# Kernel tuning notes

Measured on AMD Instinct MI355X. Metric: run time of the kernel, lower is better.

Reference implementation:

```python
import jax, jax.numpy as jnp
import numpy as np
from math import factorial as fact

L, P, T, CIN, COUT, N = 4, 5, 15, 32, 32, 1000


def _cg(j1, m1, j2, m2, J, M):
    # Clebsch-Gordan coefficient <j1 m1 j2 m2 | J M> (integer args, Racah formula)
    if m1 + m2 != M or not (abs(j1 - j2) <= J <= j1 + j2):
        return 0.0
    if abs(m1) > j1 or abs(m2) > j2 or abs(M) > J:
        return 0.0
    pre = (2.0 * J + 1.0) * fact(J + j1 - j2) * fact(J - j1 + j2) * fact(j1 + j2 - J) / fact(j1 + j2 + J + 1)
    pre *= fact(J + M) * fact(J - M) * fact(j1 - m1) * fact(j1 + m1) * fact(j2 - m2) * fact(j2 + m2)
    s = 0.0
    for k in range(0, j1 + j2 - J + 1):
        d = (k, j1 + j2 - J - k, j1 - m1 - k, j2 + m2 - k, J - j2 + m1 + k, J - j1 - m2 + k)
        if min(d) < 0:
            continue
        den = 1.0
        for x in d:
            den *= fact(x)
        s += (-1.0) ** k / den
    return float(np.sqrt(pre) * s)


def _precompute(Ldeg):
    # Mirrors PrecomputingTensorsForConv6D
    tensors, coefs = [], []
    for l in range(Ldeg):
        for l1 in range(Ldeg):
            for l2 in range(abs(l - l1), min(Ldeg, l + l1 + 1)):
                coefs.append(8.0 * np.pi ** 2 / (2 * l1 + 1)
                             * np.sqrt((2 * l + 1) * (2 * l1 + 1) / (4.0 * np.pi * (2 * l2 + 1)))
                             * _cg(l, 0, l1, 0, l2, 0))
                T1 = np.zeros((l + 1, l1 + 1, l2 + 1)); T2 = np.zeros_like(T1); T3 = np.zeros_like(T1)
                for k in range(l + 1):
                    for k1 in range(l1 + 1):
                        if abs(k + k1) < l2 + 1:
                            T1[k, k1, k + k1] = _cg(l, k, l1, k1, l2, k + k1) * (-1) ** k1
                        if k1 > 0 and abs(k - k1) < l2 + 1:
                            if k - k1 >= 0:
                                T2[k, k1, k - k1] = _cg(l, k, l1, -k1, l2, k - k1) * (-1) ** l1
                            else:
                                T3[k, k1, k1 - k] = (-1) ** (k1 - k) * (-1) ** (l1 + l2) * _cg(l, k, l1, -k1, l2, k - k1)
                tensors.append((jnp.asarray(T1, jnp.float32), jnp.asarray(T2, jnp.float32), jnp.asarray(T3, jnp.float32)))
    return tensors, np.asarray(coefs, np.float64)

_TENSORS, _COEFS = _precompute(L)


def setup_inputs() -> dict:
    key = jax.random.key(0)
    ks = iter(jax.random.split(key, 64))
    inp = {}
    for l in range(L):
        inp[f"in{l}_real"] = 0.1 * jax.random.normal(next(ks), (N, T, l + 1, P, CIN), jnp.float32)
        inp[f"in{l}_imag"] = 0.1 * jax.random.normal(next(ks), (N, T, l + 1, P, CIN), jnp.float32)
    for l in range(L):
        inp[f"w{l}_real"] = 0.05 * jax.random.normal(next(ks), (l + 1, T, P, CIN, COUT), jnp.float32)
        inp[f"w{l}_imag"] = 0.05 * jax.random.normal(next(ks), (l + 1, T, P, CIN, COUT), jnp.float32)
    for l in range(L):
        inp[f"b{l}_real"] = jax.random.uniform(next(ks), (1, l + 1, P, COUT), jnp.float32, -0.05, 0.05)
        inp[f"b{l}_imag"] = jax.random.uniform(next(ks), (1, l + 1, P, COUT), jnp.float32, -0.05, 0.05)
    return inp


def _forward(ins, ws_raw, bs_raw):
    # Mask imaginary parts: weight order-0 row (k=0) and bias degree-0 component are zeroed,
    # exactly as the temp_term masks in build().
    ws, bs = [], []
    for l in range(L):
        wmask = jnp.ones((l + 1, 1, 1, 1, 1), jnp.float32).at[0].set(0.0)
        ws += [ws_raw[2 * l], ws_raw[2 * l + 1] * wmask]
        bmask = jnp.ones((1, l + 1, 1, 1), jnp.float32).at[:, 0].set(0.0)
        bs += [bs_raw[2 * l], bs_raw[2 * l + 1] * bmask]
    outputs = []
    itr = 0
    for l in range(L):
        out_r = 0.0
        out_i = 0.0
        for l1 in range(L):
            for l2 in range(abs(l - l1), min(L, l + l1 + 1)):
                c = float(_COEFS[itr])
                T1, T2, T3 = _TENSORS[itr]
                xr, xi = ins[2 * l2], ins[2 * l2 + 1]      # [N, T, l2+1, P, Cin]
                wr, wi = ws[2 * l1], ws[2 * l1 + 1]        # [l1+1, T, P, Cin, Cout]
                # complex CG contraction -> [N, l+1, P, Cout]
                out_r = out_r + c * jnp.einsum('lmk,ntkpi,mtpij->nlpj', T1 + T2 + T3, xr, wr)
                out_r = out_r - c * jnp.einsum('lmk,ntkpi,mtpij->nlpj', T1 - T2 + T3, xi, wi)
                out_i = out_i + c * jnp.einsum('lmk,ntkpi,mtpij->nlpj', T1 - T2 - T3, xr, wi)
                out_i = out_i + c * jnp.einsum('lmk,ntkpi,mtpij->nlpj', T1 + T2 - T3, xi, wr)
                itr += 1
        outputs.append(out_r + bs[2 * l])
        outputs.append(out_i + bs[2 * l + 1])
    return tuple(outputs)


def reference(in0_real, in0_imag, in1_real, in1_imag, in2_real, in2_imag, in3_real, in3_imag,
              w0_real, w0_imag, w1_real, w1_imag, w2_real, w2_imag, w3_real, w3_imag,
              b0_real, b0_imag, b1_real, b1_imag, b2_real, b2_imag, b3_real, b3_imag):
    ins = [in0_real, in0_imag, in1_real, in1_imag, in2_real, in2_imag, in3_real, in3_imag]
    ws = [w0_real, w0_imag, w1_real, w1_imag, w2_real, w2_imag, w3_real, w3_imag]
    bs = [b0_real, b0_imag, b1_real, b1_imag, b2_real, b2_imag, b3_real, b3_imag]
    return _forward(ins, ws, bs)
```

## Files before the change

kernel.cpp:

```cpp
#include <hip/hip_runtime.h>
#include <hip/hip_bf16.h>

#define NB   1000
#define NPAD 1024
#define TT   15
#define PP   5
#define CI   32
#define CO   32
#define KDIM 9600
#define MDIM 640
#define NCHUNK 300
#define NCOL   20
#define TABN  16384
#define KSTEPS 150
#define WTELEMS 1536000
#define WTRX_BLOCKS 300
#define TAB_BLOCKS (TABN / 256)
#define XSLOTS 6000000
#define PADSLOTS 144000
#define XCVT_BLOCKS 24001

typedef __attribute__((ext_vector_type(8))) short          bf16x8;
typedef __attribute__((ext_vector_type(8))) unsigned short ushort8;
typedef __attribute__((ext_vector_type(4))) float          f32x4;

struct Chunks {
  short ci[NCHUNK]; short l2[NCHUNK]; short t[NCHUNK]; short k2[NCHUNK];
  short xidx[NCHUNK]; short cls[NCHUNK]; int ns[NCHUNK]; int offc[NCHUNK];
};
constexpr Chunks mkchunks() {
  Chunks c{};
  int idx = 0;
  for (int l2 = 0; l2 < 4; ++l2)
    for (int ci = 0; ci < 2; ++ci)
      for (int t = 0; t < TT; ++t)
        for (int k2 = 0; k2 <= l2; ++k2) {
          c.ci[idx] = (short)ci; c.l2[idx] = (short)l2;
          c.t[idx] = (short)t;   c.k2[idx] = (short)k2;
          c.xidx[idx] = (short)(2 * l2 + ci);
          c.cls[idx]  = (short)(l2 * (l2 + 1) / 2 + k2);
          c.ns[idx]   = TT * (l2 + 1) * PP * CI;
          c.offc[idx] = (t * (l2 + 1) + k2) * PP * CI;
          ++idx;
        }
  return c;
}
__constant__ Chunks g_ck = mkchunks();

struct Cols { int l[NCOL]; int lm[NCOL]; int ci[NCOL]; long obase[NCOL]; };
constexpr Cols mkcols() {
  Cols c{};
  long acc = 0; int idx = 0;
  for (int l = 0; l < 4; ++l)
    for (int ci = 0; ci < 2; ++ci) {
      for (int lm = 0; lm <= l; ++lm) {
        c.l[idx] = l; c.lm[idx] = lm; c.ci[idx] = ci; c.obase[idx] = acc; ++idx;
      }
      acc += (long)NB * (l + 1) * PP * CO;
    }
  return c;
}
__constant__ Cols g_cols = mkcols();

constexpr int wtsize(int tensor) { return ((tensor >> 1) + 1) * TT * PP * CI * CO; }
struct WOffs { int off[8]; int sz[8]; };
constexpr WOffs mkwoffs() {
  WOffs w{}; int acc = 0;
  for (int i = 0; i < 8; ++i) { w.off[i] = acc; w.sz[i] = wtsize(i); acc += w.sz[i]; }
  return w;
}
__constant__ WOffs g_wo = mkwoffs();

__constant__ short g_l1of[10] = {0,1,1,2,2,2,3,3,3,3};
__constant__ short g_mof[10]  = {0,0,1,0,1,2,0,1,2,3};
__constant__ short g_wtT[20] = {0,1,2,2,3,3,4,4,4,5,5,5,6,6,6,6,7,7,7,7};
__constant__ short g_wtM[20] = {0,0,0,1,0,1,0,1,2,0,1,2,0,1,2,3,0,1,2,3};
__constant__ int   g_xslot[9] = {0,300000,600000,1200000,1800000,2700000,3600000,4800000,6000000};
__constant__ short g_cbase[8] = {0,15,30,60,90,135,180,240};

__device__ double dfact(int n) { double r = 1.0; for (int i = 2; i <= n; ++i) r *= i; return r; }

__device__ double dcg(int j1, int m1, int j2, int m2, int J, int M) {
  if (m1 + m2 != M) return 0.0;
  int lo = j1 - j2; if (lo < 0) lo = -lo;
  if (J < lo || J > j1 + j2) return 0.0;
  int am1 = m1 < 0 ? -m1 : m1, am2 = m2 < 0 ? -m2 : m2, aM = M < 0 ? -M : M;
  if (am1 > j1 || am2 > j2 || aM > J) return 0.0;
  double pre = (2.0 * J + 1.0) * dfact(J + j1 - j2) * dfact(J - j1 + j2) * dfact(j1 + j2 - J)
               / dfact(j1 + j2 + J + 1);
  pre *= dfact(J + M) * dfact(J - M) * dfact(j1 - m1) * dfact(j1 + m1) * dfact(j2 - m2) * dfact(j2 + m2);
  double s = 0.0;
  for (int k = 0; k <= j1 + j2 - J; ++k) {
    int d1 = j1 + j2 - J - k, d2 = j1 - m1 - k, d3 = j2 + m2 - k,
        d4 = J - j2 + m1 + k, d5 = J - j1 - m2 + k;
    if (d1 < 0 || d2 < 0 || d3 < 0 || d4 < 0 || d5 < 0) continue;
    double den = dfact(k) * dfact(d1) * dfact(d2) * dfact(d3) * dfact(d4) * dfact(d5);
    s += ((k & 1) ? -1.0 : 1.0) / den;
  }
  return sqrt(pre) * s;
}

struct WArgs { const float* w[8]; float* wt; float* tab; };

__global__ __launch_bounds__(256) void k_wt(WArgs A) {
  const int bx = blockIdx.x, tid = threadIdx.x;
  __shared__ float lds[5][32][33];

  if (bx < WTRX_BLOCKS) {
    int t_ = bx % TT;
    int mrow = bx / TT;
    int tensor = g_wtT[mrow], m = g_wtM[mrow];
    const float* src = A.w[tensor] + (size_t)(m * TT + t_) * (PP * CI * CO);
    #pragma unroll
    for (int k = 0; k < 5; ++k) {
      int f = tid + k * 256;
      float4 v = *(const float4*)(src + f * 4);
      int elem = f * 4;
      int p = elem >> 10, rem = elem & 1023;
      int i = rem >> 5, j0 = rem & 31;
      lds[p][i][j0] = v.x; lds[p][i][j0 + 1] = v.y;
      lds[p][i][j0 + 2] = v.z; lds[p][i][j0 + 3] = v.w;
    }
    __syncthreads();
    float* dst = A.wt + g_wo.off[tensor] + (size_t)m * (PP * CO * TT * CI) + t_ * CI;
    #pragma unroll
    for (int k = 0; k < 20; ++k) {
      int e = tid + k * 256;
      int i = e & 31, pj = e >> 5;
      dst[pj * (TT * CI) + i] = lds[pj >> 5][i][pj & 31];
    }
  } else {
    int idx = (bx - WTRX_BLOCKS) * 256 + tid;
    int k2 = idx & 3, m = (idx >> 2) & 3, lm = (idx >> 4) & 3, l2 = (idx >> 6) & 3,
        l1 = (idx >> 8) & 3, l = (idx >> 10) & 3, combo = (idx >> 12) & 3;
    float v = 0.f;
    int dlo = l - l1; if (dlo < 0) dlo = -dlo;
    bool valid = (lm <= l) && (m <= l1) && (k2 <= l2) && (l2 >= dlo) && (l2 <= l + l1);
    if (valid) {
      const double PI = 3.14159265358979323846;
      double coef = 8.0 * PI * PI / (2.0 * l1 + 1.0)
                    * sqrt((2.0 * l + 1.0) * (2.0 * l1 + 1.0) / (4.0 * PI * (2.0 * l2 + 1.0)))
                    * dcg(l, 0, l1, 0, l2, 0);
      double t1 = 0.0, t2 = 0.0, t3 = 0.0;
      if (k2 == lm + m)
        t1 = dcg(l, lm, l1, m, l2, k2) * ((m & 1) ? -1.0 : 1.0);
      if (m > 0 && lm - m >= 0 && k2 == lm - m)
        t2 = dcg(l, lm, l1, -m, l2, lm - m) * ((l1 & 1) ? -1.0 : 1.0);
      if (m > 0 && lm - m < 0 && k2 == m - lm)
        t3 = (((m - lm) & 1) ? -1.0 : 1.0) * (((l1 + l2) & 1) ? -1.0 : 1.0)
             * dcg(l, lm, l1, -m, l2, lm - m);
      double r = 0.0;
      if (combo == 0) r =  coef * (t1 + t2 + t3);
      else if (combo == 1) r = -coef * (t1 - t2 + t3);
      else if (combo == 2) r =  coef * (t1 - t2 - t3);
      else r = coef * (t1 + t2 - t3);
      v = (float)r;
    }
    A.tab[idx] = v;
  }
}

struct XArgs { const float* x[8]; unsigned short* xb; };

__global__ __launch_bounds__(256) void k_xcvt(XArgs A) {
  int g = blockIdx.x * 256 + threadIdx.x;
  if (g >= XSLOTS) {
    int g2 = g - XSLOTS;
    if (g2 >= PADSLOTS) return;
    int pi = g2 % 1200;
    int rest = g2 / 1200;
    int n = 1000 + rest % 24, p = rest / 24;
    ushort8 z = {0,0,0,0,0,0,0,0};
    *(ushort8*)(A.xb + ((size_t)(p * NPAD + n)) * KDIM + pi * 8) = z;
    return;
  }
  int tensor = 0;
  #pragma unroll
  for (int q = 1; q < 8; ++q) if (g >= g_xslot[q]) tensor = q;
  int le = g - g_xslot[tensor];
  int l2 = tensor >> 1;
  int i8 = le & 3;
  int rem = le >> 2;
  int p = rem % PP;
  int rem2 = rem / PP;
  int k2, rem3;
  switch (l2) {
    case 0:  k2 = 0;          rem3 = rem2;      break;
    case 1:  k2 = rem2 & 1;   rem3 = rem2 >> 1; break;
    case 2:  k2 = rem2 % 3;   rem3 = rem2 / 3;  break;
    default: k2 = rem2 & 3;   rem3 = rem2 >> 2; break;
  }
  int t = rem3 % TT;
  int n = rem3 / TT;
  int chunk = g_cbase[tensor] + t * (l2 + 1) + k2;

  const float* src = A.x[tensor] + (size_t)le * 8;
  float4 a = *(const float4*)src;
  float4 b = *(const float4*)(src + 4);
  float fa[8] = {a.x, a.y, a.z, a.w, b.x, b.y, b.z, b.w};
  ushort8 o;
  #pragma unroll
  for (int e = 0; e < 8; ++e) {
    unsigned u = __float_as_uint(fa[e]);
    u += 0x7fff + ((u >> 16) & 1);
    o[e] = (unsigned short)(u >> 16);
  }
  *(ushort8*)(A.xb + ((size_t)(p * NPAD + n)) * KDIM + chunk * 32 + i8 * 8) = o;
}

struct FArgs { const float* wt; const float* tab; unsigned short* weffT; };

__global__ __launch_bounds__(256) void k_fold(FArgs A) {
  const int tid = threadIdx.x;
  const int mo = blockIdx.x, p = blockIdx.y;
  const int j = mo & 31, col = mo >> 5;
  const int l = g_cols.l[col], lm = g_cols.lm[col], cio = g_cols.ci[col];
  __shared__ float ldsW[2][10][480];
  __shared__ float ldsC[2][10][10];

  for (int e = tid; e < 2 * 10 * 480; e += 256) {
    int ti = e % 480;
    int rowid = e / 480;
    int wci = rowid / 10, r = rowid % 10;
    int l1 = g_l1of[r], m = g_mof[r];
    ldsW[wci][r][ti] = A.wt[g_wo.off[2 * l1 + wci] + m * (PP * CO * TT * CI)
                            + (p * CO + j) * (TT * CI) + ti];
  }
  if (tid < 200) {
    int r = tid % 10, clk = (tid / 10) % 10, ci = tid / 100;
    int l1 = g_l1of[r], m = g_mof[r];
    int l2 = g_l1of[clk], k2 = g_mof[clk];
    int combo = cio * 2 + ci, wci = cio ^ ci;
    float v = 0.f;
    int dlo = l - l1; if (dlo < 0) dlo = -dlo;
    if (l2 >= dlo && l2 <= l + l1 && m <= l1 && k2 <= l2)
      v = A.tab[(((((combo * 4 + l) * 4 + l1) * 4 + l2) * 4 + lm) * 4 + m) * 4 + k2];
    if (wci == 1 && m == 0) v = 0.f;
    ldsC[ci][clk][r] = v;
  }
  __syncthreads();

  unsigned short* dst = A.weffT + ((size_t)(p * MDIM + mo)) * KDIM;
  for (int s = tid; s < KDIM / 8; s += 256) {
    int chunk = s >> 2, i0 = (s & 3) * 8;
    int ci = g_ck.ci[chunk], t = g_ck.t[chunk], cls = g_ck.cls[chunk];
    int wci = cio ^ ci;
    float acc8[8] = {};
    #pragma unroll
    for (int r = 0; r < 10; ++r) {
      float c = ldsC[ci][cls][r];
      const float* wrow = &ldsW[wci][r][t * 32 + i0];
      #pragma unroll
      for (int e = 0; e < 8; ++e) acc8[e] += c * wrow[e];
    }
    ushort8 o;
    #pragma unroll
    for (int e = 0; e < 8; ++e) {
      unsigned u = __float_as_uint(acc8[e]);
      u += 0x7fff + ((u >> 16) & 1);
      o[e] = (unsigned short)(u >> 16);
    }
    *(ushort8*)(dst + s * 8) = o;
  }
}

__device__ __forceinline__ void gl_lds16(const void* g, void* l) {
  __builtin_amdgcn_global_load_lds(
      (const __attribute__((address_space(1))) unsigned int*)g,
      (__attribute__((address_space(3))) unsigned int*)l, 16, 0, 0);
}

struct GArgs { const unsigned short* xb; const unsigned short* weffT; float* partial; int nsplit; };

__global__ __launch_bounds__(256, 4) void k_gemm(GArgs A) {
  const int tid = threadIdx.x;
  const int lane = tid & 63;
  const int wv = tid >> 6, wr = wv >> 1, wc = wv & 1;
  const int NS = A.nsplit;

  const int x = blockIdx.x & 7;
  const int jj = blockIdx.x >> 3;
  const int perx = 25 * NS;
  const int full = perx / 40;
  int zz, slot;
  if (jj < full * 40) { zz = x + 8 * (jj / 40); slot = jj % 40; }
  else {
    int leftover = perx - full * 40;
    int idx = x * leftover + (jj - full * 40);
    zz = full * 8 + idx / 40; slot = idx % 40;
  }
  const int n0 = (slot & 7) * 128, mo0 = (slot >> 3) * 128;
  const int p = zz / NS, sp = zz % NS;
  const int bsteps = KSTEPS / NS, rem = KSTEPS % NS;
  const int mysteps = bsteps + (sp < rem ? 1 : 0);
  const int sstart = sp * bsteps + (sp < rem ? sp : rem);

  __shared__ __align__(16) unsigned short sA[128 * 64];
  __shared__ __align__(16) unsigned short sB[128 * 64];
  f32x4 acc[4][4] = {};

  int aoff[4];
  #pragma unroll
  for (int u = 0; u < 4; ++u) {
    int s = u * 256 + tid;
    int row = s >> 3;
    int qs = (s & 7) ^ (row & 7);
    aoff[u] = row * KDIM + qs * 8;
  }
  const unsigned short* xbase = A.xb + (size_t)p * NPAD * KDIM + (size_t)n0 * KDIM + sstart * 64;
  const unsigned short* wbase = A.weffT + (size_t)p * MDIM * KDIM + (size_t)mo0 * KDIM + sstart * 64;

  for (int cc = 0; cc < mysteps; ++cc) {
    const unsigned short* xs = xbase + cc * 64;
    const unsigned short* ws = wbase + cc * 64;
    #pragma unroll
    for (int u = 0; u < 4; ++u) {
      gl_lds16(xs + aoff[u], (void*)(sA + (u * 256 + tid) * 8));
      gl_lds16(ws + aoff[u], (void*)(sB + (u * 256 + tid) * 8));
    }
    __syncthreads();
    #pragma unroll
    for (int ks = 0; ks < 2; ++ks) {
      const int q = ks * 4 + (lane >> 4);
      bf16x8 af[4], bfr[4];
      #pragma unroll
      for (int m = 0; m < 4; ++m) {
        int ra = wr * 64 + m * 16 + (lane & 15);
        af[m] = *(const bf16x8*)(sA + ra * 64 + ((q ^ (ra & 7)) << 3));
      }
      #pragma unroll
      for (int n = 0; n < 4; ++n) {
        int rb = wc * 64 + n * 16 + (lane & 15);
        bfr[n] = *(const bf16x8*)(sB + rb * 64 + ((q ^ (rb & 7)) << 3));
      }
      #pragma unroll
      for (int m = 0; m < 4; ++m)
        #pragma unroll
        for (int n = 0; n < 4; ++n)
          acc[m][n] = __builtin_amdgcn_mfma_f32_16x16x32_bf16(af[m], bfr[n], acc[m][n], 0, 0, 0);
    }
    __syncthreads();
  }

  float* pout = A.partial + (size_t)zz * (NPAD * MDIM);
  #pragma unroll
  for (int m = 0; m < 4; ++m) {
    #pragma unroll
    for (int nn = 0; nn < 4; ++nn) {
      int mo = mo0 + wc * 64 + nn * 16 + (lane & 15);
      #pragma unroll
      for (int r = 0; r < 4; ++r) {
        int n = n0 + wr * 64 + m * 16 + (lane >> 4) * 4 + r;
        pout[(size_t)n * MDIM + mo] = acc[m][nn][r];
      }
    }
  }
}

struct RArgs { const float* partial; const float* b[8]; float* out; int nsplit; };

__global__ __launch_bounds__(256) void k_red(RArgs A) {
  int e4 = blockIdx.x * 256 + threadIdx.x;
  if (e4 >= NB * (MDIM / 4) * PP) return;
  int mo4 = e4 % (MDIM / 4);
  int rest = e4 / (MDIM / 4);
  int n = rest % NB;
  int p = rest / NB;
  int mo = mo4 * 4;
  float4 s = make_float4(0.f, 0.f, 0.f, 0.f);
  for (int sp = 0; sp < A.nsplit; ++sp) {
    float4 v = *(const float4*)&A.partial[((size_t)(p * A.nsplit + sp) * NPAD + n) * MDIM + mo];
    s.x += v.x; s.y += v.y; s.z += v.z; s.w += v.w;
  }
  int colid = mo >> 5, j = mo & 31;
  int l = g_cols.l[colid], lmv = g_cols.lm[colid], cio = g_cols.ci[colid];
  long base = g_cols.obase[colid];
  float4 bias = *(const float4*)&A.b[2 * l + cio][(lmv * PP + p) * CO + j];
  if (cio == 1 && lmv == 0) bias = make_float4(0.f, 0.f, 0.f, 0.f);
  float4 o = make_float4(s.x + bias.x, s.y + bias.y, s.z + bias.z, s.w + bias.w);
  *(float4*)&A.out[base + (((size_t)n * (l + 1) + lmv) * PP + p) * CO + j] = o;
}

extern "C" void kernel_launch(void* const* d_in, const int* in_sizes, int n_in,
                              void* d_out, int out_size, void* d_ws, size_t ws_size,
                              hipStream_t stream) {
  float* tab = (float*)d_ws;
  float* wt  = tab + TABN;
  unsigned short* weffT = (unsigned short*)(wt + WTELEMS);
  unsigned short* xb    = weffT + (size_t)PP * MDIM * KDIM;
  float* partial = (float*)(xb + (size_t)PP * NPAD * KDIM);

  size_t base_bytes = (size_t)TABN * 4 + (size_t)WTELEMS * 4
                    + (size_t)PP * MDIM * KDIM * 2 + (size_t)PP * NPAD * KDIM * 2;
  size_t per_split = (size_t)PP * NPAD * MDIM * 4;
  int NS = 1;
  for (int c = 5; c >= 2; --c)
    if (ws_size >= base_bytes + (size_t)c * per_split) { NS = c; break; }

  WArgs wa;
  for (int i = 0; i < 8; ++i) wa.w[i] = (const float*)d_in[8 + i];
  wa.wt = wt; wa.tab = tab;
  k_wt<<<dim3(WTRX_BLOCKS + TAB_BLOCKS), dim3(256), 0, stream>>>(wa);

  XArgs xa;
  for (int i = 0; i < 8; ++i) xa.x[i] = (const float*)d_in[i];
  xa.xb = xb;
  k_xcvt<<<dim3(XCVT_BLOCKS), dim3(256), 0, stream>>>(xa);

  FArgs fa;
  fa.wt = wt; fa.tab = (const float*)tab; fa.weffT = weffT;
  k_fold<<<dim3(MDIM, PP), dim3(256), 0, stream>>>(fa);

  GArgs ga;
  ga.xb = xb; ga.weffT = weffT; ga.partial = partial; ga.nsplit = NS;
  k_gemm<<<dim3(200 * NS), dim3(256), 0, stream>>>(ga);

  RArgs ra;
  ra.partial = partial; ra.out = (float*)d_out; ra.nsplit = NS;
  for (int i = 0; i < 8; ++i) ra.b[i] = (const float*)d_in[16 + i];
  k_red<<<dim3((NB * (MDIM / 4) * PP + 255) / 256), dim3(256), 0, stream>>>(ra);
}
```

Before: 219.7 us.

## Use 256x256 GEMM tiles with double-buffered LDS and 512-thread blocks

New measurement: 230.0 us. +4.7%, slower.

```diff
diff --git a/kernel.cpp b/kernel.cpp
--- a/kernel.cpp
+++ b/kernel.cpp
@@ -9,6 +9,7 @@
 #define CO   32
 #define KDIM 9600
 #define MDIM 640
+#define MPAD 768
 #define NCHUNK 300
 #define NCOL   20
 #define TABN  16384
@@ -272,37 +273,32 @@
 
 struct GArgs { const unsigned short* xb; const unsigned short* weffT; float* partial; int nsplit; };
 
-__global__ __launch_bounds__(256, 4) void k_gemm(GArgs A) {
+__global__ __launch_bounds__(512, 2) void k_gemm(GArgs A) {
   const int tid = threadIdx.x;
   const int lane = tid & 63;
-  const int wv = tid >> 6, wr = wv >> 1, wc = wv & 1;
+  const int wv = tid >> 6;
+  const int wr = wv >> 2;
+  const int wc = wv & 3;
   const int NS = A.nsplit;
 
-  const int x = blockIdx.x & 7;
-  const int jj = blockIdx.x >> 3;
-  const int perx = 25 * NS;
-  const int full = perx / 40;
-  int zz, slot;
-  if (jj < full * 40) { zz = x + 8 * (jj / 40); slot = jj % 40; }
-  else {
-    int leftover = perx - full * 40;
-    int idx = x * leftover + (jj - full * 40);
-    zz = full * 8 + idx / 40; slot = idx % 40;
-  }
-  const int n0 = (slot & 7) * 128, mo0 = (slot >> 3) * 128;
+  const int nwg = 60 * NS;
+  const int per = nwg >> 3;
+  const int wgid = (blockIdx.x & 7) * per + (blockIdx.x >> 3);
+  const int zz = wgid / 12, slot = wgid % 12;
+  const int n0 = (slot & 3) * 256, mo0 = (slot >> 2) * 256;
   const int p = zz / NS, sp = zz % NS;
   const int bsteps = KSTEPS / NS, rem = KSTEPS % NS;
   const int mysteps = bsteps + (sp < rem ? 1 : 0);
   const int sstart = sp * bsteps + (sp < rem ? sp : rem);
 
-  __shared__ __align__(16) unsigned short sA[128 * 64];
-  __shared__ __align__(16) unsigned short sB[128 * 64];
-  f32x4 acc[4][4] = {};
+  __shared__ __align__(16) unsigned short sA[2][256 * 64];
+  __shared__ __align__(16) unsigned short sB[2][256 * 64];
+  f32x4 acc[8][4] = {};
 
   int aoff[4];
   #pragma unroll
   for (int u = 0; u < 4; ++u) {
-    int s = u * 256 + tid;
+    int s = u * 512 + tid;
     int row = s >> 3;
     int qs = (s & 7) ^ (row & 7);
     aoff[u] = row * KDIM + qs * 8;
@@ -310,51 +306,73 @@
   const unsigned short* xbase = A.xb + (size_t)p * NPAD * KDIM + (size_t)n0 * KDIM + sstart * 64;
   const unsigned short* wbase = A.weffT + (size_t)p * MDIM * KDIM + (size_t)mo0 * KDIM + sstart * 64;
 
-  for (int cc = 0; cc < mysteps; ++cc) {
-    const unsigned short* xs = xbase + cc * 64;
-    const unsigned short* ws = wbase + cc * 64;
-    #pragma unroll
-    for (int u = 0; u < 4; ++u) {
-      gl_lds16(xs + aoff[u], (void*)(sA + (u * 256 + tid) * 8));
-      gl_lds16(ws + aoff[u], (void*)(sB + (u * 256 + tid) * 8));
-    }
-    __syncthreads();
-    #pragma unroll
-    for (int ks = 0; ks < 2; ++ks) {
-      const int q = ks * 4 + (lane >> 4);
-      bf16x8 af[4], bfr[4];
-      #pragma unroll
-      for (int m = 0; m < 4; ++m) {
-        int ra = wr * 64 + m * 16 + (lane & 15);
-        af[m] = *(const bf16x8*)(sA + ra * 64 + ((q ^ (ra & 7)) << 3));
-      }
-      #pragma unroll
-      for (int n = 0; n < 4; ++n) {
-        int rb = wc * 64 + n * 16 + (lane & 15);
-        bfr[n] = *(const bf16x8*)(sB + rb * 64 + ((q ^ (rb & 7)) << 3));
-      }
-      #pragma unroll
-      for (int m = 0; m < 4; ++m)
-        #pragma unroll
-        for (int n = 0; n < 4; ++n)
-          acc[m][n] = __builtin_amdgcn_mfma_f32_16x16x32_bf16(af[m], bfr[n], acc[m][n], 0, 0, 0);
-    }
-    __syncthreads();
+#define STG(BUF, step) {                                                            \
+    const unsigned short* xs = xbase + (size_t)(step) * 64;                         \
+    const unsigned short* ws = wbase + (size_t)(step) * 64;                         \
+    _Pragma("unroll")                                                               \
+    for (int u = 0; u < 4; ++u)                                                     \
+      gl_lds16(xs + aoff[u], (void*)(&sA[BUF][(u * 512 + tid) * 8]));               \
+    _Pragma("unroll")                                                               \
+    for (int u = 0; u < 4; ++u)                                                     \
+      gl_lds16(ws + aoff[u], (void*)(&sB[BUF][(u * 512 + tid) * 8]));               \
+  }
+
+#define CMP(BUF) {                                                                  \
+    _Pragma("unroll")                                                               \
+    for (int ks = 0; ks < 2; ++ks) {                                                \
+      const int q = ks * 4 + (lane >> 4);                                           \
+      bf16x8 af[8], bfr[4];                                                         \
+      _Pragma("unroll")                                                             \
+      for (int m = 0; m < 8; ++m) {                                                 \
+        int ra = wr * 128 + m * 16 + (lane & 15);                                   \
+        af[m] = *(const bf16x8*)&sA[BUF][ra * 64 + ((q ^ (ra & 7)) << 3)];          \
+      }                                                                             \
+      _Pragma("unroll")                                                             \
+      for (int n = 0; n < 4; ++n) {                                                 \
+        int rb = wc * 64 + n * 16 + (lane & 15);                                    \
+        bfr[n] = *(const bf16x8*)&sB[BUF][rb * 64 + ((q ^ (rb & 7)) << 3)];         \
+      }                                                                             \
+      _Pragma("unroll")                                                             \
+      for (int m = 0; m < 8; ++m)                                                   \
+        _Pragma("unroll")                                                           \
+        for (int n = 0; n < 4; ++n)                                                 \
+          acc[m][n] = __builtin_amdgcn_mfma_f32_16x16x32_bf16(af[m], bfr[n],        \
+                                                              acc[m][n], 0, 0, 0);  \
+    }                                                                               \
+  }
+
+  STG(0, 0);
+  if (mysteps > 1) STG(1, 1);
+  for (int t = 0; t < mysteps; ++t) {
+    const int cur = t & 1;
+    if (t + 1 < mysteps) asm volatile("s_waitcnt vmcnt(8)" ::: "memory");
+    else                 asm volatile("s_waitcnt vmcnt(0)" ::: "memory");
+    __builtin_amdgcn_s_barrier();
+    asm volatile("" ::: "memory");
+    CMP(cur);
+    asm volatile("" ::: "memory");
+    __builtin_amdgcn_s_barrier();
+    asm volatile("" ::: "memory");
+    if (t + 2 < mysteps) STG(cur, t + 2);
   }
 
   float* pout = A.partial + (size_t)zz * (NPAD * MDIM);
   #pragma unroll
-  for (int m = 0; m < 4; ++m) {
+  for (int m = 0; m < 8; ++m) {
     #pragma unroll
     for (int nn = 0; nn < 4; ++nn) {
       int mo = mo0 + wc * 64 + nn * 16 + (lane & 15);
-      #pragma unroll
-      for (int r = 0; r < 4; ++r) {
-        int n = n0 + wr * 64 + m * 16 + (lane >> 4) * 4 + r;
-        pout[(size_t)n * MDIM + mo] = acc[m][nn][r];
+      if (mo < MDIM) {
+        #pragma unroll
+        for (int r = 0; r < 4; ++r) {
+          int n = n0 + wr * 128 + m * 16 + (lane >> 4) * 4 + r;
+          pout[(size_t)n * MDIM + mo] = acc[m][nn][r];
+        }
       }
     }
   }
+#undef STG
+#undef CMP
 }
 
 struct RArgs { const float* partial; const float* b[8]; float* out; int nsplit; };
@@ -393,9 +411,8 @@
   size_t base_bytes = (size_t)TABN * 4 + (size_t)WTELEMS * 4
                     + (size_t)PP * MDIM * KDIM * 2 + (size_t)PP * NPAD * KDIM * 2;
   size_t per_split = (size_t)PP * NPAD * MDIM * 4;
-  int NS = 1;
-  for (int c = 5; c >= 2; --c)
-    if (ws_size >= base_bytes + (size_t)c * per_split) { NS = c; break; }
+  int NS = 2;
+  if (ws_size >= base_bytes + 4 * per_split) NS = 4;
 
   WArgs wa;
   for (int i = 0; i < 8; ++i) wa.w[i] = (const float*)d_in[8 + i];
@@ -413,7 +430,7 @@
 
   GArgs ga;
   ga.xb = xb; ga.weffT = weffT; ga.partial = partial; ga.nsplit = NS;
-  k_gemm<<<dim3(200 * NS), dim3(256), 0, stream>>>(ga);
+  k_gemm<<<dim3(60 * NS), dim3(512), 0, stream>>>(ga);
 
   RArgs ra;
   ra.partial = partial; ra.out = (float*)d_out; ra.nsplit = NS;
```
